# Performance work log

Hardware: AMD Instinct MI355X
Metric: run time of the kernel (lower is better)

Reference implementation:

```python
import jax, jax.numpy as jnp
import numpy as np
from jax import lax

T, H, I, E, K = 1024, 1024, 512, 16, 4


def setup_inputs() -> dict:
    key = jax.random.key(0)
    k1, k2, k3, k4, k5 = jax.random.split(key, 5)
    hidden_states = jax.random.normal(k1, (T, H), dtype=jnp.float32)
    top_k_index = jax.random.randint(k2, (T, K), 0, E)
    top_k_weights = jax.random.uniform(k3, (T, K), dtype=jnp.float32)
    gate_up_proj = jax.random.normal(k4, (E, 2 * I, H), dtype=jnp.float32) * 0.02
    down_proj = jax.random.normal(k5, (E, H, I), dtype=jnp.float32) * 0.02
    return {
        "hidden_states": hidden_states,
        "top_k_index": top_k_index,
        "top_k_weights": top_k_weights,
        "gate_up_proj": gate_up_proj,
        "down_proj": down_proj,
    }


def reference(hidden_states, top_k_index, top_k_weights, gate_up_proj, down_proj):
    num_experts = gate_up_proj.shape[0]
    # combine[t, e] = sum_k top_k_weights[t, k] * [top_k_index[t, k] == e]
    # Expert output is linear in the routing weight, so summing weights over
    # duplicate (token, expert) hits matches the original index_add_ exactly.
    one_hot = jax.nn.one_hot(top_k_index, num_experts, dtype=hidden_states.dtype)  # [T, K, E]
    combine = jnp.einsum("tke,tk->te", one_hot, top_k_weights)  # [T, E]

    def expert_step(acc, xs):
        w_gu, w_d, c = xs  # [2I, H], [H, I], [T]
        gu = hidden_states @ w_gu.T          # [T, 2I]
        gate, up = jnp.split(gu, 2, axis=-1)
        h = jax.nn.silu(gate) * up            # [T, I]
        out = h @ w_d.T                       # [T, H]
        return acc + out * c[:, None], None

    final, _ = lax.scan(
        expert_step,
        jnp.zeros_like(hidden_states),
        (gate_up_proj, down_proj, combine.T),
    )
    return final
```

## Files before the change

kernel.cpp:

```cpp
#include <hip/hip_runtime.h>
#include <hip/hip_bf16.h>
#include <cstdint>
#include <cstddef>

#define T_TOK 1024
#define HDIM  1024
#define IDIM  512
#define NEXP  16
#define TOPK  4
#define CAP   1024

typedef __bf16 bf16;
typedef __attribute__((ext_vector_type(8))) __bf16 bf16x8;
typedef __attribute__((ext_vector_type(4))) __bf16 bf16x4;
typedef __attribute__((ext_vector_type(4))) float f32x4;

__device__ __forceinline__ void lds_load16(void* lds_dst, const void* g_src) {
  __builtin_amdgcn_global_load_lds(
      (__attribute__((address_space(1))) unsigned int*)(void*)(g_src),
      (__attribute__((address_space(3))) unsigned int*)(lds_dst),
      16, 0, 0);
}

__device__ __forceinline__ bf16x4 cvt4(float4 a) {
  bf16x4 o;
  o[0] = (bf16)a.x; o[1] = (bf16)a.y; o[2] = (bf16)a.z; o[3] = (bf16)a.w;
  return o;
}


#define CVT_BLOCKS (T_TOK * HDIM / 4 / 256)

__global__ void prep_kernel(const float* __restrict__ hid_f, bf16* __restrict__ hid_b,
                            const int* __restrict__ idx, const float* __restrict__ w,
                            int* __restrict__ etk, float* __restrict__ ew,
                            int* __restrict__ cntpad) {
  __shared__ int cnt;
  const int b = blockIdx.x;
  const int tid = threadIdx.x;
  if (b < CVT_BLOCKS) {
    int i = b * 256 + tid;
    float4 v = ((const float4*)hid_f)[i];
    ((bf16x4*)hid_b)[i] = cvt4(v);
    if (b == 0)
      ((bf16x4*)(hid_b + (size_t)T_TOK * HDIM))[tid] = cvt4(make_float4(0.f, 0.f, 0.f, 0.f));
    return;
  }
  const int e = b - CVT_BLOCKS;
  if (tid == 0) cnt = 0;
  __syncthreads();
  for (int j = tid; j < T_TOK * TOPK; j += blockDim.x) {
    if (idx[j] == e) {
      int slot = atomicAdd(&cnt, 1);
      if (slot < CAP) { etk[e * CAP + slot] = j; ew[e * CAP + slot] = w[j]; }
    }
  }
  __syncthreads();
  int c = cnt < CAP ? cnt : CAP;
  int p = (c + 127) & ~127;
  for (int j = c + tid; j < p; j += blockDim.x) {
    etk[e * CAP + j] = (T_TOK << 2);
    ew[e * CAP + j] = 0.f;
  }
  if (tid == 0) cntpad[e] = p;
}


__global__ __launch_bounds__(256, 3) void gemm1_kernel(
    const bf16* __restrict__ hid,
    const float* __restrict__ gup,
    const int* __restrict__ etk, const float* __restrict__ ew,
    const int* __restrict__ cntpad,
    bf16* __restrict__ hsc) {
  __shared__ __align__(16) bf16 As[2][128 * 64];
  __shared__ __align__(16) bf16 Bs[2][64 * 64];
  const int e = blockIdx.y, z = blockIdx.z;
  const int ntiles = cntpad[e] >> 7;
  const int n0 = blockIdx.x * 32;
  const int ebase = e * CAP;
  const int tid = threadIdx.x, lane = tid & 63, wid = tid >> 6;
  const int wm = (wid >> 1) * 64, wi = (wid & 1) * 16;
  const int lcol = lane & 15, lquad = lane >> 4;
  const int l7 = lcol & 7;
  const int srow = tid >> 3;
  const int swz = ((tid & 7) ^ (srow & 7)) * 8;
  const int r = tid >> 2;
  const int c0 = (tid & 3) * 4;
  const int grow = (r < 32) ? (n0 + r) : (IDIM + n0 + (r - 32));
  const float* gB = gup + (size_t)e * (2 * IDIM) * HDIM + (size_t)grow * HDIM + c0;
  int wb[4];
#pragma unroll
  for (int j = 0; j < 4; ++j) {
    int c = c0 + 16 * j;
    wb[j] = (((c >> 3) ^ (r & 7)) * 8) + (c & 7);
  }
  const int bst = r * 64;

  for (int mt = z; mt < ntiles; mt += 3) {
    const int mrow = ebase + mt * 128;
    const bf16* gA[4];
#pragma unroll
    for (int q = 0; q < 4; ++q)
      gA[q] = hid + (size_t)(etk[mrow + srow + 32 * q] >> 2) * HDIM + swz;
    f32x4 aG[4], aU[4];
#pragma unroll
    for (int mf = 0; mf < 4; ++mf) {
      aG[mf] = f32x4{0.f, 0.f, 0.f, 0.f};
      aU[mf] = f32x4{0.f, 0.f, 0.f, 0.f};
    }
    {
      float4 bv[4];
#pragma unroll
      for (int j = 0; j < 4; ++j) bv[j] = *(const float4*)(gB + 16 * j);
#pragma unroll
      for (int q = 0; q < 4; ++q)
        lds_load16(&As[0][tid * 8 + q * 2048], gA[q]);
#pragma unroll
      for (int j = 0; j < 4; ++j)
        *(bf16x4*)&Bs[0][bst + wb[j]] = cvt4(bv[j]);
    }
    __syncthreads();
#pragma unroll 2
    for (int k = 0; k < 16; ++k) {
      const int cur = k & 1, nxt = cur ^ 1;
      float4 bn[4];
      if (k < 15) {
#pragma unroll
        for (int q = 0; q < 4; ++q)
          lds_load16(&As[nxt][tid * 8 + q * 2048], gA[q] + (k + 1) * 64);
#pragma unroll
        for (int j = 0; j < 4; ++j)
          bn[j] = *(const float4*)(gB + (k + 1) * 64 + 16 * j);
      }
#pragma unroll
      for (int ks = 0; ks < 2; ++ks) {
        const int lch = ks * 4 + lquad;
        const int sw = (lch ^ l7) * 8;
        bf16x8 bg = *(const bf16x8*)&Bs[cur][(wi + lcol) * 64 + sw];
        bf16x8 bu = *(const bf16x8*)&Bs[cur][(32 + wi + lcol) * 64 + sw];
#pragma unroll
        for (int mf = 0; mf < 4; ++mf) {
          bf16x8 af = *(const bf16x8*)&As[cur][(wm + mf * 16 + lcol) * 64 + sw];
          aG[mf] = __builtin_amdgcn_mfma_f32_16x16x32_bf16(af, bg, aG[mf], 0, 0, 0);
          aU[mf] = __builtin_amdgcn_mfma_f32_16x16x32_bf16(af, bu, aU[mf], 0, 0, 0);
        }
      }
      if (k < 15) {
#pragma unroll
        for (int j = 0; j < 4; ++j)
          *(bf16x4*)&Bs[nxt][bst + wb[j]] = cvt4(bn[j]);
      }
      __syncthreads();
    }
#pragma unroll
    for (int mf = 0; mf < 4; ++mf) {
#pragma unroll
      for (int rr = 0; rr < 4; ++rr) {
        const int erow = mt * 128 + wm + mf * 16 + lquad * 4 + rr;
        const float wgt = ew[ebase + erow];
        float g = aG[mf][rr], u = aU[mf][rr];
        float s = g / (1.f + __expf(-g));
        hsc[(size_t)(ebase + erow) * IDIM + n0 + wi + lcol] = (bf16)(s * u * wgt);
      }
    }
  }
}


__global__ __launch_bounds__(256, 3) void gemm2_kernel(
    const bf16* __restrict__ hsc,
    const float* __restrict__ down,
    const int* __restrict__ etk, const int* __restrict__ cntpad,
    float* __restrict__ slabs) {
  __shared__ __align__(16) bf16 As[2][128 * 64];
  __shared__ __align__(16) bf16 Bs[2][64 * 64];
  const int e = blockIdx.y, z = blockIdx.z;
  const int ntiles = cntpad[e] >> 7;
  const int n0 = blockIdx.x * 64;
  const int ebase = e * CAP;
  const int tid = threadIdx.x, lane = tid & 63, wid = tid >> 6;
  const int wm = (wid >> 1) * 64, wh = (wid & 1) * 32;
  const int lcol = lane & 15, lquad = lane >> 4;
  const int l7 = lcol & 7;
  const int srow = tid >> 3;
  const int swz = ((tid & 7) ^ (srow & 7)) * 8;
  const int r = tid >> 2;
  const int c0 = (tid & 3) * 4;
  const float* gB = down + (size_t)e * HDIM * IDIM + (size_t)(n0 + r) * IDIM + c0;
  int wb[4];
#pragma unroll
  for (int j = 0; j < 4; ++j) {
    int c = c0 + 16 * j;
    wb[j] = (((c >> 3) ^ (r & 7)) * 8) + (c & 7);
  }
  const int bst = r * 64;

  for (int mt = z; mt < ntiles; mt += 3) {
    const size_t rbase = (size_t)(ebase + mt * 128);
    const bf16* gA[4];
#pragma unroll
    for (int q = 0; q < 4; ++q)
      gA[q] = hsc + (rbase + srow + 32 * q) * IDIM + swz;
    f32x4 acc[4][2];
#pragma unroll
    for (int mf = 0; mf < 4; ++mf) {
      acc[mf][0] = f32x4{0.f, 0.f, 0.f, 0.f};
      acc[mf][1] = f32x4{0.f, 0.f, 0.f, 0.f};
    }
    {
      float4 bv[4];
#pragma unroll
      for (int j = 0; j < 4; ++j) bv[j] = *(const float4*)(gB + 16 * j);
#pragma unroll
      for (int q = 0; q < 4; ++q)
        lds_load16(&As[0][tid * 8 + q * 2048], gA[q]);
#pragma unroll
      for (int j = 0; j < 4; ++j)
        *(bf16x4*)&Bs[0][bst + wb[j]] = cvt4(bv[j]);
    }
    __syncthreads();
#pragma unroll 2
    for (int k = 0; k < 8; ++k) {
      const int cur = k & 1, nxt = cur ^ 1;
      float4 bn[4];
      if (k < 7) {
#pragma unroll
        for (int q = 0; q < 4; ++q)
          lds_load16(&As[nxt][tid * 8 + q * 2048], gA[q] + (k + 1) * 64);
#pragma unroll
        for (int j = 0; j < 4; ++j)
          bn[j] = *(const float4*)(gB + (k + 1) * 64 + 16 * j);
      }
#pragma unroll
      for (int ks = 0; ks < 2; ++ks) {
        const int lch = ks * 4 + lquad;
        const int sw = (lch ^ l7) * 8;
        bf16x8 b0 = *(const bf16x8*)&Bs[cur][(wh + lcol) * 64 + sw];
        bf16x8 b1 = *(const bf16x8*)&Bs[cur][(wh + 16 + lcol) * 64 + sw];
#pragma unroll
        for (int mf = 0; mf < 4; ++mf) {
          bf16x8 af = *(const bf16x8*)&As[cur][(wm + mf * 16 + lcol) * 64 + sw];
          acc[mf][0] = __builtin_amdgcn_mfma_f32_16x16x32_bf16(af, b0, acc[mf][0], 0, 0, 0);
          acc[mf][1] = __builtin_amdgcn_mfma_f32_16x16x32_bf16(af, b1, acc[mf][1], 0, 0, 0);
        }
      }
      if (k < 7) {
#pragma unroll
        for (int j = 0; j < 4; ++j)
          *(bf16x4*)&Bs[nxt][bst + wb[j]] = cvt4(bn[j]);
      }
      __syncthreads();
    }
#pragma unroll
    for (int mf = 0; mf < 4; ++mf) {
#pragma unroll
      for (int rr = 0; rr < 4; ++rr) {
        const int row = mt * 128 + wm + mf * 16 + lquad * 4 + rr;
        const int tk = etk[ebase + row];
        const int tok = tk >> 2, ksl = tk & 3;
        float* orow = slabs + ((size_t)ksl * (T_TOK + 1) + tok) * HDIM + n0 + wh + lcol;
        orow[0] = acc[mf][0][rr];
        orow[16] = acc[mf][1][rr];
      }
    }
  }
}


__global__ void reduce_kernel(const float* __restrict__ slabs, float* __restrict__ out) {
  const size_t stride = (size_t)(T_TOK + 1) * HDIM;
  int i = blockIdx.x * blockDim.x + threadIdx.x;
  float4 a = ((const float4*)slabs)[i];
  float4 b = ((const float4*)(slabs + stride))[i];
  float4 c = ((const float4*)(slabs + 2 * stride))[i];
  float4 d = ((const float4*)(slabs + 3 * stride))[i];
  float4 o;
  o.x = a.x + b.x + c.x + d.x;
  o.y = a.y + b.y + c.y + d.y;
  o.z = a.z + b.z + c.z + d.z;
  o.w = a.w + b.w + c.w + d.w;
  ((float4*)out)[i] = o;
}


extern "C" void kernel_launch(void* const* d_in, const int* in_sizes, int n_in,
                              void* d_out, int out_size, void* d_ws, size_t ws_size,
                              hipStream_t stream) {
  const float* hid_f  = (const float*)d_in[0];
  const int*   idx    = (const int*)d_in[1];
  const float* tw     = (const float*)d_in[2];
  const float* gup_f  = (const float*)d_in[3];
  const float* down_f = (const float*)d_in[4];
  float* out = (float*)d_out;

  uint8_t* ws = (uint8_t*)d_ws;
  size_t off = 0;
  bf16* hid_b = (bf16*)(ws + off);   off += (size_t)(T_TOK + 1) * HDIM * 2;
  int*  etk   = (int*)(ws + off);    off += (size_t)NEXP * CAP * 4;
  float* ewt  = (float*)(ws + off);  off += (size_t)NEXP * CAP * 4;
  int* cntpad = (int*)(ws + off);    off += 256;
  bf16* hsc   = (bf16*)(ws + off);   off += (size_t)NEXP * CAP * IDIM * 2;
  float* slabs = (float*)(ws + off);

  prep_kernel<<<dim3(CVT_BLOCKS + NEXP), dim3(256), 0, stream>>>(
      hid_f, hid_b, idx, tw, etk, ewt, cntpad);
  gemm1_kernel<<<dim3(IDIM / 32, NEXP, 3), dim3(256), 0, stream>>>(
      hid_b, gup_f, etk, ewt, cntpad, hsc);
  gemm2_kernel<<<dim3(HDIM / 64, NEXP, 3), dim3(256), 0, stream>>>(
      hsc, down_f, etk, cntpad, slabs);
  reduce_kernel<<<dim3(T_TOK * HDIM / 4 / 256), dim3(256), 0, stream>>>(slabs, out);
}
```

Before: 172.5 us.

## Scatter down-proj results with atomics into output, drop slab reduce kernel

The second GEMM now accumulates each expert's contribution directly into the output with float atomicAdd, and the output is zeroed inside the prep kernel. This removes the four per-k-slot slabs and the separate reduce kernel, along with their write/read traffic and one launch. The MFMA inner loops are also wrapped in s_setprio raises to favour compute waves. The trade-off is atomic contention, since up to four experts hit the same row, and a summation order that is no longer deterministic.

```diff
diff --git a/kernel.cpp b/kernel.cpp
--- a/kernel.cpp
+++ b/kernel.cpp
@@ -34,7 +34,7 @@
 __global__ void prep_kernel(const float* __restrict__ hid_f, bf16* __restrict__ hid_b,
                             const int* __restrict__ idx, const float* __restrict__ w,
                             int* __restrict__ etk, float* __restrict__ ew,
-                            int* __restrict__ cntpad) {
+                            int* __restrict__ cntpad, float* __restrict__ out) {
   __shared__ int cnt;
   const int b = blockIdx.x;
   const int tid = threadIdx.x;
@@ -42,6 +42,7 @@
     int i = b * 256 + tid;
     float4 v = ((const float4*)hid_f)[i];
     ((bf16x4*)hid_b)[i] = cvt4(v);
+    ((float4*)out)[i] = make_float4(0.f, 0.f, 0.f, 0.f);
     if (b == 0)
       ((bf16x4*)(hid_b + (size_t)T_TOK * HDIM))[tid] = cvt4(make_float4(0.f, 0.f, 0.f, 0.f));
     return;
@@ -132,6 +133,7 @@
         for (int j = 0; j < 4; ++j)
           bn[j] = *(const float4*)(gB + (k + 1) * 64 + 16 * j);
       }
+      __builtin_amdgcn_s_setprio(1);
 #pragma unroll
       for (int ks = 0; ks < 2; ++ks) {
         const int lch = ks * 4 + lquad;
@@ -145,6 +147,7 @@
           aU[mf] = __builtin_amdgcn_mfma_f32_16x16x32_bf16(af, bu, aU[mf], 0, 0, 0);
         }
       }
+      __builtin_amdgcn_s_setprio(0);
       if (k < 15) {
 #pragma unroll
         for (int j = 0; j < 4; ++j)
@@ -171,7 +174,7 @@
     const bf16* __restrict__ hsc,
     const float* __restrict__ down,
     const int* __restrict__ etk, const int* __restrict__ cntpad,
-    float* __restrict__ slabs) {
+    float* __restrict__ out) {
   __shared__ __align__(16) bf16 As[2][128 * 64];
   __shared__ __align__(16) bf16 Bs[2][64 * 64];
   const int e = blockIdx.y, z = blockIdx.z;
@@ -231,6 +234,7 @@
         for (int j = 0; j < 4; ++j)
           bn[j] = *(const float4*)(gB + (k + 1) * 64 + 16 * j);
       }
+      __builtin_amdgcn_s_setprio(1);
 #pragma unroll
       for (int ks = 0; ks < 2; ++ks) {
         const int lch = ks * 4 + lquad;
@@ -244,6 +248,7 @@
           acc[mf][1] = __builtin_amdgcn_mfma_f32_16x16x32_bf16(af, b1, acc[mf][1], 0, 0, 0);
         }
       }
+      __builtin_amdgcn_s_setprio(0);
       if (k < 7) {
 #pragma unroll
         for (int j = 0; j < 4; ++j)
@@ -257,29 +262,15 @@
       for (int rr = 0; rr < 4; ++rr) {
         const int row = mt * 128 + wm + mf * 16 + lquad * 4 + rr;
         const int tk = etk[ebase + row];
-        const int tok = tk >> 2, ksl = tk & 3;
-        float* orow = slabs + ((size_t)ksl * (T_TOK + 1) + tok) * HDIM + n0 + wh + lcol;
-        orow[0] = acc[mf][0][rr];
-        orow[16] = acc[mf][1][rr];
-      }
-    }
-  }
-}
-
-
-__global__ void reduce_kernel(const float* __restrict__ slabs, float* __restrict__ out) {
-  const size_t stride = (size_t)(T_TOK + 1) * HDIM;
-  int i = blockIdx.x * blockDim.x + threadIdx.x;
-  float4 a = ((const float4*)slabs)[i];
-  float4 b = ((const float4*)(slabs + stride))[i];
-  float4 c = ((const float4*)(slabs + 2 * stride))[i];
-  float4 d = ((const float4*)(slabs + 3 * stride))[i];
-  float4 o;
-  o.x = a.x + b.x + c.x + d.x;
-  o.y = a.y + b.y + c.y + d.y;
-  o.z = a.z + b.z + c.z + d.z;
-  o.w = a.w + b.w + c.w + d.w;
-  ((float4*)out)[i] = o;
+        const int tok = tk >> 2;
+        if (tok < T_TOK) {
+          float* orow = out + (size_t)tok * HDIM + n0 + wh + lcol;
+          atomicAdd(orow, acc[mf][0][rr]);
+          atomicAdd(orow + 16, acc[mf][1][rr]);
+        }
+      }
+    }
+  }
 }
 
 
@@ -299,14 +290,12 @@
   int*  etk   = (int*)(ws + off);    off += (size_t)NEXP * CAP * 4;
   float* ewt  = (float*)(ws + off);  off += (size_t)NEXP * CAP * 4;
   int* cntpad = (int*)(ws + off);    off += 256;
-  bf16* hsc   = (bf16*)(ws + off);   off += (size_t)NEXP * CAP * IDIM * 2;
-  float* slabs = (float*)(ws + off);
+  bf16* hsc   = (bf16*)(ws + off);
 
   prep_kernel<<<dim3(CVT_BLOCKS + NEXP), dim3(256), 0, stream>>>(
-      hid_f, hid_b, idx, tw, etk, ewt, cntpad);
+      hid_f, hid_b, idx, tw, etk, ewt, cntpad, out);
   gemm1_kernel<<<dim3(IDIM / 32, NEXP, 3), dim3(256), 0, stream>>>(
       hid_b, gup_f, etk, ewt, cntpad, hsc);
   gemm2_kernel<<<dim3(HDIM / 64, NEXP, 3), dim3(256), 0, stream>>>(
-      hsc, down_f, etk, cntpad, slabs);
-  reduce_kernel<<<dim3(T_TOK * HDIM / 4 / 256), dim3(256), 0, stream>>>(slabs, out);
-}
+      hsc, down_f, etk, cntpad, out);
+}
```

Measured after the change: 176.9 us. 1.03x slower.
